# Optimization experiments

Hardware: AMD Instinct MI355X
Metric: run time of the kernel (lower is better)

## Reference

```python
import jax, jax.numpy as jnp
import numpy as np

B, N, S, D1, D2 = 16, 4096, 1024, 128, 256
MLP = [256, 128]
BN_EPS = 1e-5


def setup_inputs() -> dict:
    key = jax.random.key(0)
    ks = jax.random.split(key, 12)
    inp = {
        "xyz1": jax.random.normal(ks[0], (B, 3, N), dtype=jnp.float32),
        "xyz2": jax.random.normal(ks[1], (B, 3, S), dtype=jnp.float32),
        "points1": jax.random.normal(ks[2], (B, D1, N), dtype=jnp.float32),
        "points2": jax.random.normal(ks[3], (B, D2, S), dtype=jnp.float32),
    }
    in_ch = D1 + D2  # 384
    chans = [in_ch] + MLP
    ki = 4
    for li in range(len(MLP)):
        cin, cout = chans[li], chans[li + 1]
        inp[f"w{li+1}"] = jax.random.normal(ks[ki], (cout, cin), dtype=jnp.float32) * (1.0 / np.sqrt(cin)); ki += 1
        inp[f"b{li+1}"] = jnp.zeros((cout,), dtype=jnp.float32)
        inp[f"g{li+1}"] = jnp.ones((cout,), dtype=jnp.float32)
        inp[f"beta{li+1}"] = jnp.zeros((cout,), dtype=jnp.float32)
    return inp


def _batchnorm1d(x, gamma, beta):
    # x: [B, C, N]; training-mode batch stats over (B, N)
    mean = jnp.mean(x, axis=(0, 2), keepdims=True)
    var = jnp.var(x, axis=(0, 2), keepdims=True)
    xhat = (x - mean) * jax.lax.rsqrt(var + BN_EPS)
    return xhat * gamma[None, :, None] + beta[None, :, None]


def reference(xyz1, xyz2, points1, points2, w1, b1, g1, beta1, w2, b2, g2, beta2):
    x1 = jnp.transpose(xyz1, (0, 2, 1))   # [B, N, 3]
    x2 = jnp.transpose(xyz2, (0, 2, 1))   # [B, S, 3]
    p2 = jnp.transpose(points2, (0, 2, 1))  # [B, S, D2]

    # squared pairwise distances [B, N, S]
    dists = jnp.sum((x1[:, :, None, :] - x2[:, None, :, :]) ** 2, axis=-1)
    # 3 smallest distances (original sorts then slices top-3)
    neg_d3, idx = jax.lax.top_k(-dists, 3)  # [B, N, 3]
    d3 = -neg_d3
    dist_recip = 1.0 / (d3 + 1e-8)
    weight = dist_recip / jnp.sum(dist_recip, axis=2, keepdims=True)  # [B, N, 3]

    # gather neighbor features: [B, N, 3, D2]
    feats = p2[jnp.arange(p2.shape[0])[:, None, None], idx]
    interp = jnp.sum(feats * weight[..., None], axis=2)  # [B, N, D2]

    p1 = jnp.transpose(points1, (0, 2, 1))  # [B, N, D1]
    new_points = jnp.concatenate([p1, interp], axis=-1)  # [B, N, D1+D2]
    x = jnp.transpose(new_points, (0, 2, 1))  # [B, C, N]

    for w, b, g, bt in ((w1, b1, g1, beta1), (w2, b2, g2, beta2)):
        x = jnp.einsum("oc,bcn->bon", w, x) + b[None, :, None]
        x = _batchnorm1d(x, g, bt)
        x = jax.nn.relu(x)
    return x
```

## Files before the change

### kernel.cpp

```cpp
#include <hip/hip_runtime.h>

typedef unsigned short u16;
typedef unsigned int   u32;
typedef unsigned long long u64;
typedef __attribute__((ext_vector_type(8))) short bf16x8;
typedef __attribute__((ext_vector_type(8))) unsigned short u16x8;
typedef __attribute__((ext_vector_type(4))) float f32x4;

#define NB   16
#define NPTS 4096
#define SPTS 1024
#define BNT  65536

#define G2L(src, dst) __builtin_amdgcn_global_load_lds( \
    (const __attribute__((address_space(1))) void*)(src), \
    (__attribute__((address_space(3))) void*)(dst), 16, 0, 0)

__device__ __forceinline__ float bf2f(u16 u){ return __uint_as_float(((u32)u)<<16); }
__device__ __forceinline__ u16 f2bf(float f){
  u32 u = __float_as_uint(f);
  return (u16)((u + 0x7FFFu + ((u>>16)&1u))>>16);
}

__global__ __launch_bounds__(256) void convw_k(const float* __restrict__ w1, const float* __restrict__ w2,
                                               u16* __restrict__ w1b, u16* __restrict__ w2b){
  int i = blockIdx.x*256 + threadIdx.x;
  if (i < 98304) w1b[i] = f2bf(w1[i]);
  else { int j = i - 98304; w2b[j] = f2bf(w2[j]); }
}

__global__ __launch_bounds__(256) void transpose_k(const float* __restrict__ in, u16* __restrict__ out,
                                                   int C, int S, int ostride){
  __shared__ float tl[64][65];
  int t = threadIdx.x;
  int b = blockIdx.y;
  int s0 = blockIdx.x * 64;
  for (int ct = 0; ct < C; ct += 64){
    __syncthreads();
    for (int i = t; i < 4096; i += 256){
      int sl = i & 63, cl = i >> 6;
      tl[sl][cl] = in[((size_t)b*C + ct + cl)*S + s0 + sl];
    }
    __syncthreads();
    for (int i = t; i < 4096; i += 256){
      int cl = i & 63, sl = i >> 6;
      out[((size_t)b*S + s0 + sl)*ostride + ct + cl] = f2bf(tl[sl][cl]);
    }
  }
}

__global__ __launch_bounds__(512) void knn_k(const float* __restrict__ xyz1, const float* __restrict__ xyz2,
                                             const u16* __restrict__ p2t, u16* __restrict__ X){
  __shared__ float4 sxyz[SPTS];
  __shared__ double pp[8][3][64];
  __shared__ float  swts[3][64];
  __shared__ int    sidx[3][64];
  int t  = threadIdx.x;
  int b  = blockIdx.x >> 6;
  int n0 = (blockIdx.x & 63) << 6;
  const float* x2b = xyz2 + (size_t)b*3*SPTS;
  for (int s = t; s < SPTS; s += 512)
    sxyz[s] = make_float4(x2b[s], x2b[SPTS+s], x2b[2*SPTS+s], 0.f);
  int q = t & 63, g = t >> 6;
  const float* x1b = xyz1 + (size_t)b*3*NPTS;
  int n = n0 + q;
  float qx = x1b[n], qy = x1b[NPTS+n], qz = x1b[2*NPTS+n];
  __syncthreads();

  double k0 = 1e300, k1 = 1e300, k2 = 1e300;
  int sBeg = g << 7;
  #pragma unroll 4
  for (int sj = 0; sj < 128; ++sj){
    int s = sBeg + sj;
    float4 p = sxyz[s];
    float dist;
    {
      #pragma clang fp contract(off)
      float dx = qx - p.x, dy = qy - p.y, dz = qz - p.z;
      dist = ((dx*dx) + (dy*dy)) + (dz*dz);
    }
    double pk = __longlong_as_double(__double_as_longlong((double)dist) | (long long)s);
    double n2 = fmin(fmax(pk, k1), k2);
    double n1 = fmin(fmax(pk, k0), k1);
    double n0d = fmin(pk, k0);
    k0 = n0d; k1 = n1; k2 = n2;
  }
  pp[g][0][q] = k0; pp[g][1][q] = k1; pp[g][2][q] = k2;
  __syncthreads();

  if (t < 64){
    double m0 = 1e300, m1 = 1e300, m2 = 1e300;
    #pragma unroll
    for (int gg = 0; gg < 8; ++gg){
      #pragma unroll
      for (int p = 0; p < 3; ++p){
        double pk = pp[gg][p][t];
        double n2 = fmin(fmax(pk, m1), m2);
        double n1 = fmin(fmax(pk, m0), m1);
        double n0d = fmin(pk, m0);
        m0 = n0d; m1 = n1; m2 = n2;
      }
    }
    int j0 = (int)(__double_as_longlong(m0) & 1023);
    int j1 = (int)(__double_as_longlong(m1) & 1023);
    int j2 = (int)(__double_as_longlong(m2) & 1023);
    float e0 = (float)m0, e1 = (float)m1, e2 = (float)m2;
    float r0 = 1.f/(e0 + 1e-8f), r1 = 1.f/(e1 + 1e-8f), r2 = 1.f/(e2 + 1e-8f);
    float rs = (r0 + r1) + r2;
    swts[0][t] = r0/rs; swts[1][t] = r1/rs; swts[2][t] = r2/rs;
    sidx[0][t] = j0;    sidx[1][t] = j1;    sidx[2][t] = j2;
  }
  __syncthreads();

  int w = t >> 6, lane = t & 63;
  for (int qq = w*8; qq < w*8 + 8; ++qq){
    float wa = swts[0][qq], wb = swts[1][qq], wc = swts[2][qq];
    int   j0 = sidx[0][qq], j1 = sidx[1][qq], j2 = sidx[2][qq];
    const ushort4 u0 = *(const ushort4*)(p2t + (((size_t)b*SPTS + j0)<<8) + (lane<<2));
    const ushort4 u1 = *(const ushort4*)(p2t + (((size_t)b*SPTS + j1)<<8) + (lane<<2));
    const ushort4 u2 = *(const ushort4*)(p2t + (((size_t)b*SPTS + j2)<<8) + (lane<<2));
    ushort4 ov;
    ov.x = f2bf(wa*bf2f(u0.x) + wb*bf2f(u1.x) + wc*bf2f(u2.x));
    ov.y = f2bf(wa*bf2f(u0.y) + wb*bf2f(u1.y) + wc*bf2f(u2.y));
    ov.z = f2bf(wa*bf2f(u0.z) + wb*bf2f(u1.z) + wc*bf2f(u2.z));
    ov.w = f2bf(wa*bf2f(u0.w) + wb*bf2f(u1.w) + wc*bf2f(u2.w));
    *(ushort4*)(X + ((size_t)b*NPTS + n0 + qq)*384 + 128 + (lane<<2)) = ov;
  }
}

__global__ __launch_bounds__(256) void gemm1_k(const u16* __restrict__ A, const u16* __restrict__ Bw,
                                               u16* __restrict__ Cc,
                                               float* __restrict__ psum, float* __restrict__ psq){
  const int K = 384, Nn = 256;
  __shared__ u16 lA[2][64*64];
  __shared__ u16 lB[2][256*64];
  __shared__ float sums[256], sqs[256];
  int t = threadIdx.x, lane = t & 63, wid = t >> 6;
  int rowBase = blockIdx.x << 6;
  int wm = wid >> 1, wn = wid & 1;

  const char* pA[2]; int dAo[2];
  #pragma unroll
  for (int j = 0; j < 2; ++j){
    int L = j*4096 + t*16;
    int row = L >> 7, kb = L & 127;
    int kbs = kb ^ ((row & 7) << 4);
    pA[j] = (const char*)A + ((size_t)(rowBase + row)*K)*2 + kbs;
    dAo[j] = j*4096 + wid*1024;
  }
  const char* pB[8]; int dBo[8];
  #pragma unroll
  for (int j = 0; j < 8; ++j){
    int L = j*4096 + t*16;
    int row = L >> 7, kb = L & 127;
    int kbs = kb ^ ((row & 7) << 4);
    pB[j] = (const char*)Bw + ((size_t)row*K)*2 + kbs;
    dBo[j] = j*4096 + wid*1024;
  }

  f32x4 z = {0.f,0.f,0.f,0.f};
  f32x4 acc[2][8];
  #pragma unroll
  for (int m = 0; m < 2; ++m)
    #pragma unroll
    for (int n = 0; n < 8; ++n) acc[m][n] = z;

  #pragma unroll
  for (int j = 0; j < 2; ++j) G2L(pA[j], (char*)lA[0] + dAo[j]);
  #pragma unroll
  for (int j = 0; j < 8; ++j) G2L(pB[j], (char*)lB[0] + dBo[j]);
  __syncthreads();

  #pragma unroll
  for (int kt = 0; kt < 6; ++kt){
    const int cur = kt & 1;
    if (kt < 5){
      size_t ko = (size_t)(kt + 1) * 128;
      #pragma unroll
      for (int j = 0; j < 2; ++j) G2L(pA[j] + ko, (char*)lA[cur^1] + dAo[j]);
      #pragma unroll
      for (int j = 0; j < 8; ++j) G2L(pB[j] + ko, (char*)lB[cur^1] + dBo[j]);
    }
    #pragma unroll
    for (int ks = 0; ks < 2; ++ks){
      bf16x8 af[2];
      #pragma unroll
      for (int m = 0; m < 2; ++m){
        int row = wm*32 + m*16 + (lane & 15);
        int sw = (row & 7) << 4;
        int kb = (ks*64 + ((lane >> 4) << 4)) ^ sw;
        af[m] = *(const bf16x8*)((const char*)lA[cur] + row*128 + kb);
      }
      #pragma unroll
      for (int n = 0; n < 8; ++n){
        int row = wn*128 + n*16 + (lane & 15);
        int sw = (row & 7) << 4;
        int kb = (ks*64 + ((lane >> 4) << 4)) ^ sw;
        bf16x8 bv = *(const bf16x8*)((const char*)lB[cur] + row*128 + kb);
        #pragma unroll
        for (int m = 0; m < 2; ++m)
          acc[m][n] = __builtin_amdgcn_mfma_f32_16x16x32_bf16(af[m], bv, acc[m][n], 0, 0, 0);
      }
    }
    __syncthreads();
  }

  sums[t] = 0.f; sqs[t] = 0.f;
  __syncthreads();
  int colb = wn*128 + (lane & 15);
  int rowb = rowBase + wm*32 + ((lane >> 4) << 2);
  #pragma unroll
  for (int n = 0; n < 8; ++n){
    float s = 0.f, qq2 = 0.f;
    #pragma unroll
    for (int m = 0; m < 2; ++m){
      #pragma unroll
      for (int r = 0; r < 4; ++r){
        float v = acc[m][n][r];
        Cc[(size_t)(rowb + m*16 + r)*Nn + colb + n*16] = f2bf(v);
        s += v; qq2 += v*v;
      }
    }
    atomicAdd(&sums[colb + n*16], s);
    atomicAdd(&sqs [colb + n*16], qq2);
  }
  __syncthreads();
  psum[(size_t)t*1024 + blockIdx.x] = sums[t];
  psq [(size_t)t*1024 + blockIdx.x] = sqs[t];
}

__global__ __launch_bounds__(256) void gemm2_k(const u16* __restrict__ A, const u16* __restrict__ Bw,
                                               u16* __restrict__ Cc,
                                               const float* __restrict__ sc, const float* __restrict__ sh,
                                               float* __restrict__ psum, float* __restrict__ psq){
  const int K = 256, Nn = 128;
  __shared__ u16 lA[2][64*64];
  __shared__ u16 lB[2][128*64];
  __shared__ float sums[128], sqs[128];
  int t = threadIdx.x, lane = t & 63, wid = t >> 6;
  int rowBase = blockIdx.x << 6;
  int wm = wid >> 1, wn = wid & 1;

  const char* pB[4]; int dBo[4];
  #pragma unroll
  for (int j = 0; j < 4; ++j){
    int L = j*4096 + t*16;
    int row = L >> 7, kb = L & 127;
    int kbs = kb ^ ((row & 7) << 4);
    pB[j] = (const char*)Bw + ((size_t)row*K)*2 + kbs;
    dBo[j] = j*4096 + wid*1024;
  }
  int arow = t & 63, achunk = t >> 6;
  const u16* pArow = A + (size_t)(rowBase + arow)*K + achunk*16;
  int asw = (arow & 7) << 4;
  int wAo0 = arow*128 + ((achunk*32)      ^ asw);
  int wAo1 = arow*128 + ((achunk*32 + 16) ^ asw);

  f32x4 z = {0.f,0.f,0.f,0.f};
  f32x4 acc[2][4];
  #pragma unroll
  for (int m = 0; m < 2; ++m)
    #pragma unroll
    for (int n = 0; n < 4; ++n) acc[m][n] = z;

  #pragma unroll
  for (int j = 0; j < 4; ++j) G2L(pB[j], (char*)lB[0] + dBo[j]);
  {
    u16x8 y0 = *(const u16x8*)(pArow);
    u16x8 y1 = *(const u16x8*)(pArow + 8);
    int k0 = achunk*16;
    bf16x8 o0, o1;
    #pragma unroll
    for (int j = 0; j < 8; ++j){
      float v = bf2f((u16)y0[j]) * sc[k0 + j] + sh[k0 + j];
      o0[j] = (short)f2bf(fmaxf(v, 0.f));
    }
    #pragma unroll
    for (int j = 0; j < 8; ++j){
      float v = bf2f((u16)y1[j]) * sc[k0 + 8 + j] + sh[k0 + 8 + j];
      o1[j] = (short)f2bf(fmaxf(v, 0.f));
    }
    *(bf16x8*)((char*)lA[0] + wAo0) = o0;
    *(bf16x8*)((char*)lA[0] + wAo1) = o1;
  }
  __syncthreads();

  #pragma unroll
  for (int kt = 0; kt < 4; ++kt){
    const int cur = kt & 1;
    u16x8 ny0 = {}, ny1 = {};
    if (kt < 3){
      size_t ko = (size_t)(kt + 1) * 128;
      #pragma unroll
      for (int j = 0; j < 4; ++j) G2L(pB[j] + ko, (char*)lB[cur^1] + dBo[j]);
      ny0 = *(const u16x8*)(pArow + (kt+1)*64);
      ny1 = *(const u16x8*)(pArow + (kt+1)*64 + 8);
    }
    #pragma unroll
    for (int ks = 0; ks < 2; ++ks){
      bf16x8 af[2];
      #pragma unroll
      for (int m = 0; m < 2; ++m){
        int row = wm*32 + m*16 + (lane & 15);
        int sw = (row & 7) << 4;
        int kb = (ks*64 + ((lane >> 4) << 4)) ^ sw;
        af[m] = *(const bf16x8*)((const char*)lA[cur] + row*128 + kb);
      }
      #pragma unroll
      for (int n = 0; n < 4; ++n){
        int row = wn*64 + n*16 + (lane & 15);
        int sw = (row & 7) << 4;
        int kb = (ks*64 + ((lane >> 4) << 4)) ^ sw;
        bf16x8 bv = *(const bf16x8*)((const char*)lB[cur] + row*128 + kb);
        #pragma unroll
        for (int m = 0; m < 2; ++m)
          acc[m][n] = __builtin_amdgcn_mfma_f32_16x16x32_bf16(af[m], bv, acc[m][n], 0, 0, 0);
      }
    }
    if (kt < 3){
      int k0 = (kt+1)*64 + achunk*16;
      bf16x8 o0, o1;
      #pragma unroll
      for (int j = 0; j < 8; ++j){
        float v = bf2f((u16)ny0[j]) * sc[k0 + j] + sh[k0 + j];
        o0[j] = (short)f2bf(fmaxf(v, 0.f));
      }
      #pragma unroll
      for (int j = 0; j < 8; ++j){
        float v = bf2f((u16)ny1[j]) * sc[k0 + 8 + j] + sh[k0 + 8 + j];
        o1[j] = (short)f2bf(fmaxf(v, 0.f));
      }
      *(bf16x8*)((char*)lA[cur^1] + wAo0) = o0;
      *(bf16x8*)((char*)lA[cur^1] + wAo1) = o1;
    }
    __syncthreads();
  }

  if (t < 128){ sums[t] = 0.f; sqs[t] = 0.f; }
  __syncthreads();
  int colb = wn*64 + (lane & 15);
  int rowb = rowBase + wm*32 + ((lane >> 4) << 2);
  #pragma unroll
  for (int n = 0; n < 4; ++n){
    float s = 0.f, qq2 = 0.f;
    #pragma unroll
    for (int m = 0; m < 2; ++m){
      #pragma unroll
      for (int r = 0; r < 4; ++r){
        float v = acc[m][n][r];
        Cc[(size_t)(rowb + m*16 + r)*Nn + colb + n*16] = f2bf(v);
        s += v; qq2 += v*v;
      }
    }
    atomicAdd(&sums[colb + n*16], s);
    atomicAdd(&sqs [colb + n*16], qq2);
  }
  __syncthreads();
  if (t < 128){
    psum[(size_t)t*1024 + blockIdx.x] = sums[t];
    psq [(size_t)t*1024 + blockIdx.x] = sqs[t];
  }
}

__global__ __launch_bounds__(256) void finalize2_k(const float* __restrict__ psum, const float* __restrict__ psq,
                                                   const float* __restrict__ g, const float* __restrict__ bet,
                                                   float* __restrict__ sc, float* __restrict__ sh){
  __shared__ float rs[256], rq[256];
  int c = blockIdx.x, t = threadIdx.x;
  float s = 0.f, q = 0.f;
  for (int rt = t; rt < 1024; rt += 256){
    s += psum[(size_t)c*1024 + rt];
    q += psq [(size_t)c*1024 + rt];
  }
  rs[t] = s; rq[t] = q;
  __syncthreads();
  for (int off = 128; off; off >>= 1){
    if (t < off){ rs[t] += rs[t+off]; rq[t] += rq[t+off]; }
    __syncthreads();
  }
  if (t == 0){
    const float inv = 1.f/65536.f;
    float mean = rs[0]*inv;
    float var  = rq[0]*inv - mean*mean;
    float rstd = rsqrtf(var + 1e-5f);
    float scl  = g[c]*rstd;
    sc[c] = scl;
    sh[c] = bet[c] - mean*scl;
  }
}

__global__ __launch_bounds__(256) void finalout_k(const u16* __restrict__ y2, const float* __restrict__ sc,
                                                  const float* __restrict__ sh, float* __restrict__ out){
  __shared__ float tl[128][65];
  int t  = threadIdx.x;
  int b  = blockIdx.x >> 6;
  int n0 = (blockIdx.x & 63) << 6;
  for (int i = t; i < 8192; i += 256){
    int r = i >> 7, c = i & 127;
    float v = bf2f(y2[((size_t)b*NPTS + n0 + r)*128 + c]);
    v = fmaxf(v*sc[c] + sh[c], 0.f);
    tl[c][r] = v;
  }
  __syncthreads();
  for (int i = t; i < 8192; i += 256){
    int o = i >> 6, j = i & 63;
    out[(size_t)b*128*NPTS + (size_t)o*NPTS + n0 + j] = tl[o][j];
  }
}

extern "C" void kernel_launch(void* const* d_in, const int* in_sizes, int n_in,
                              void* d_out, int out_size, void* d_ws, size_t ws_size,
                              hipStream_t stream) {
  const float* xyz1    = (const float*)d_in[0];
  const float* xyz2    = (const float*)d_in[1];
  const float* points1 = (const float*)d_in[2];
  const float* points2 = (const float*)d_in[3];
  const float* w1      = (const float*)d_in[4];
  const float* g1      = (const float*)d_in[6];
  const float* beta1   = (const float*)d_in[7];
  const float* w2      = (const float*)d_in[8];
  const float* g2      = (const float*)d_in[10];
  const float* beta2   = (const float*)d_in[11];

  char* ws = (char*)d_ws;
  u16*  X    = (u16*)ws;
  u16*  Y2   = (u16*)ws;
  u16*  Y1   = (u16*)(ws + 50331648);
  u16*  p2t  = (u16*)(ws + 83886080);
  u16*  w1b  = (u16*)(ws + 92274688);
  u16*  w2b  = (u16*)(ws + 92471296);
  float* psum1 = (float*)(ws + 83886080);
  float* psq1  = (float*)(ws + 84934656);
  float* psum2 = (float*)(ws + 85983232);
  float* psq2  = (float*)(ws + 86507520);
  float* sc1   = (float*)(ws + 87031808);
  float* sh1   = (float*)(ws + 87032832);
  float* sc2   = (float*)(ws + 87033856);
  float* sh2   = (float*)(ws + 87034368);

  convw_k<<<512, 256, 0, stream>>>(w1, w2, w1b, w2b);
  transpose_k<<<dim3(64, 16), 256, 0, stream>>>(points1, X,   128, NPTS, 384);
  transpose_k<<<dim3(16, 16), 256, 0, stream>>>(points2, p2t, 256, SPTS, 256);
  knn_k<<<1024, 512, 0, stream>>>(xyz1, xyz2, p2t, X);
  gemm1_k<<<1024, 256, 0, stream>>>(X, w1b, Y1, psum1, psq1);
  finalize2_k<<<256, 256, 0, stream>>>(psum1, psq1, g1, beta1, sc1, sh1);
  gemm2_k<<<1024, 256, 0, stream>>>(Y1, w2b, Y2, sc1, sh1, psum2, psq2);
  finalize2_k<<<128, 256, 0, stream>>>(psum2, psq2, g2, beta2, sc2, sh2);
  finalout_k<<<1024, 256, 0, stream>>>(Y2, sc2, sh2, (float*)d_out);
}
```

Measured before the change: 174.1 us.

## Drop LDS double buffering in both GEMMs to raise occupancy

```diff
diff --git a/kernel.cpp b/kernel.cpp
--- a/kernel.cpp
+++ b/kernel.cpp
@@ -132,9 +132,10 @@
                                                u16* __restrict__ Cc,
                                                float* __restrict__ psum, float* __restrict__ psq){
   const int K = 384, Nn = 256;
-  __shared__ u16 lA[2][64*64];
-  __shared__ u16 lB[2][256*64];
-  __shared__ float sums[256], sqs[256];
+  __shared__ u16 lA[64*64];
+  __shared__ u16 lB[256*64];
+  float* sums = (float*)lA;
+  float* sqs  = (float*)(lA + 512);
   int t = threadIdx.x, lane = t & 63, wid = t >> 6;
   int rowBase = blockIdx.x << 6;
   int wm = wid >> 1, wn = wid & 1;
@@ -166,21 +167,13 @@
     for (int n = 0; n < 8; ++n) acc[m][n] = z;
 
   #pragma unroll
-  for (int j = 0; j < 2; ++j) G2L(pA[j], (char*)lA[0] + dAo[j]);
-  #pragma unroll
-  for (int j = 0; j < 8; ++j) G2L(pB[j], (char*)lB[0] + dBo[j]);
-  __syncthreads();
-
-  #pragma unroll
   for (int kt = 0; kt < 6; ++kt){
-    const int cur = kt & 1;
-    if (kt < 5){
-      size_t ko = (size_t)(kt + 1) * 128;
-      #pragma unroll
-      for (int j = 0; j < 2; ++j) G2L(pA[j] + ko, (char*)lA[cur^1] + dAo[j]);
-      #pragma unroll
-      for (int j = 0; j < 8; ++j) G2L(pB[j] + ko, (char*)lB[cur^1] + dBo[j]);
-    }
+    size_t ko = (size_t)kt * 128;
+    #pragma unroll
+    for (int j = 0; j < 2; ++j) G2L(pA[j] + ko, (char*)lA + dAo[j]);
+    #pragma unroll
+    for (int j = 0; j < 8; ++j) G2L(pB[j] + ko, (char*)lB + dBo[j]);
+    __syncthreads();
     #pragma unroll
     for (int ks = 0; ks < 2; ++ks){
       bf16x8 af[2];
@@ -189,14 +182,14 @@
         int row = wm*32 + m*16 + (lane & 15);
         int sw = (row & 7) << 4;
         int kb = (ks*64 + ((lane >> 4) << 4)) ^ sw;
-        af[m] = *(const bf16x8*)((const char*)lA[cur] + row*128 + kb);
+        af[m] = *(const bf16x8*)((const char*)lA + row*128 + kb);
       }
       #pragma unroll
       for (int n = 0; n < 8; ++n){
         int row = wn*128 + n*16 + (lane & 15);
         int sw = (row & 7) << 4;
         int kb = (ks*64 + ((lane >> 4) << 4)) ^ sw;
-        bf16x8 bv = *(const bf16x8*)((const char*)lB[cur] + row*128 + kb);
+        bf16x8 bv = *(const bf16x8*)((const char*)lB + row*128 + kb);
         #pragma unroll
         for (int m = 0; m < 2; ++m)
           acc[m][n] = __builtin_amdgcn_mfma_f32_16x16x32_bf16(af[m], bv, acc[m][n], 0, 0, 0);
@@ -234,8 +227,8 @@
                                                const float* __restrict__ sc, const float* __restrict__ sh,
                                                float* __restrict__ psum, float* __restrict__ psq){
   const int K = 256, Nn = 128;
-  __shared__ u16 lA[2][64*64];
-  __shared__ u16 lB[2][128*64];
+  __shared__ u16 lA[64*64];
+  __shared__ u16 lB[128*64];
   __shared__ float sums[128], sqs[128];
   int t = threadIdx.x, lane = t & 63, wid = t >> 6;
   int rowBase = blockIdx.x << 6;
@@ -253,8 +246,8 @@
   int arow = t & 63, achunk = t >> 6;
   const u16* pArow = A + (size_t)(rowBase + arow)*K + achunk*16;
   int asw = (arow & 7) << 4;
-  int wAo0 = arow*128 + ((achunk*32)      ^ asw);
-  int wAo1 = arow*128 + ((achunk*32 + 16) ^ asw);
+  char* wA0 = (char*)lA + arow*128 + ((achunk*32)      ^ asw);
+  char* wA1 = (char*)lA + arow*128 + ((achunk*32 + 16) ^ asw);
 
   f32x4 z = {0.f,0.f,0.f,0.f};
   f32x4 acc[2][4];
@@ -263,12 +256,13 @@
     #pragma unroll
     for (int n = 0; n < 4; ++n) acc[m][n] = z;
 
-  #pragma unroll
-  for (int j = 0; j < 4; ++j) G2L(pB[j], (char*)lB[0] + dBo[j]);
-  {
-    u16x8 y0 = *(const u16x8*)(pArow);
-    u16x8 y1 = *(const u16x8*)(pArow + 8);
-    int k0 = achunk*16;
+  for (int kk = 0; kk < K; kk += 64){
+    size_t ko = (size_t)kk * 2;
+    #pragma unroll
+    for (int j = 0; j < 4; ++j) G2L(pB[j] + ko, (char*)lB + dBo[j]);
+    u16x8 y0 = *(const u16x8*)(pArow + kk);
+    u16x8 y1 = *(const u16x8*)(pArow + kk + 8);
+    int k0 = kk + achunk*16;
     bf16x8 o0, o1;
     #pragma unroll
     for (int j = 0; j < 8; ++j){
@@ -280,59 +274,37 @@
       float v = bf2f((u16)y1[j]) * sc[k0 + 8 + j] + sh[k0 + 8 + j];
       o1[j] = (short)f2bf(fmaxf(v, 0.f));
     }
-    *(bf16x8*)((char*)lA[0] + wAo0) = o0;
-    *(bf16x8*)((char*)lA[0] + wAo1) = o1;
-  }
-  __syncthreads();
-
-  #pragma unroll
-  for (int kt = 0; kt < 4; ++kt){
-    const int cur = kt & 1;
-    u16x8 ny0 = {}, ny1 = {};
-    if (kt < 3){
-      size_t ko = (size_t)(kt + 1) * 128;
-      #pragma unroll
-      for (int j = 0; j < 4; ++j) G2L(pB[j] + ko, (char*)lB[cur^1] + dBo[j]);
-      ny0 = *(const u16x8*)(pArow + (kt+1)*64);
-      ny1 = *(const u16x8*)(pArow + (kt+1)*64 + 8);
-    }
-    #pragma unroll
-    for (int ks = 0; ks < 2; ++ks){
-      bf16x8 af[2];
-      #pragma unroll
-      for (int m = 0; m < 2; ++m){
-        int row = wm*32 + m*16 + (lane & 15);
-        int sw = (row & 7) << 4;
+    *(bf16x8*)wA0 = o0;
+    *(bf16x8*)wA1 = o1;
+    __syncthreads();
+    bf16x8 af[2][2], bfv[4][2];
+    #pragma unroll
+    for (int m = 0; m < 2; ++m){
+      int row = wm*32 + m*16 + (lane & 15);
+      int sw = (row & 7) << 4;
+      #pragma unroll
+      for (int ks = 0; ks < 2; ++ks){
         int kb = (ks*64 + ((lane >> 4) << 4)) ^ sw;
-        af[m] = *(const bf16x8*)((const char*)lA[cur] + row*128 + kb);
-      }
-      #pragma unroll
-      for (int n = 0; n < 4; ++n){
-        int row = wn*64 + n*16 + (lane & 15);
-        int sw = (row & 7) << 4;
+        af[m][ks] = *(const bf16x8*)((const char*)lA + row*128 + kb);
+      }
+    }
+    #pragma unroll
+    for (int n = 0; n < 4; ++n){
+      int row = wn*64 + n*16 + (lane & 15);
+      int sw = (row & 7) << 4;
+      #pragma unroll
+      for (int ks = 0; ks < 2; ++ks){
         int kb = (ks*64 + ((lane >> 4) << 4)) ^ sw;
-        bf16x8 bv = *(const bf16x8*)((const char*)lB[cur] + row*128 + kb);
+        bfv[n][ks] = *(const bf16x8*)((const char*)lB + row*128 + kb);
+      }
+    }
+    #pragma unroll
+    for (int ks = 0; ks < 2; ++ks)
+      #pragma unroll
+      for (int m = 0; m < 2; ++m)
         #pragma unroll
-        for (int m = 0; m < 2; ++m)
-          acc[m][n] = __builtin_amdgcn_mfma_f32_16x16x32_bf16(af[m], bv, acc[m][n], 0, 0, 0);
-      }
-    }
-    if (kt < 3){
-      int k0 = (kt+1)*64 + achunk*16;
-      bf16x8 o0, o1;
-      #pragma unroll
-      for (int j = 0; j < 8; ++j){
-        float v = bf2f((u16)ny0[j]) * sc[k0 + j] + sh[k0 + j];
-        o0[j] = (short)f2bf(fmaxf(v, 0.f));
-      }
-      #pragma unroll
-      for (int j = 0; j < 8; ++j){
-        float v = bf2f((u16)ny1[j]) * sc[k0 + 8 + j] + sh[k0 + 8 + j];
-        o1[j] = (short)f2bf(fmaxf(v, 0.f));
-      }
-      *(bf16x8*)((char*)lA[cur^1] + wAo0) = o0;
-      *(bf16x8*)((char*)lA[cur^1] + wAo1) = o1;
-    }
+        for (int n = 0; n < 4; ++n)
+          acc[m][n] = __builtin_amdgcn_mfma_f32_16x16x32_bf16(af[m][ks], bfv[n][ks], acc[m][n], 0, 0, 0);
     __syncthreads();
   }
 
```

Result: faster. 153.5 us (-11.8%).
